# Performance work log

Hardware: AMD Instinct MI355X
Metric: run time of the kernel (lower is better)

Reference implementation:

```python
import jax, jax.numpy as jnp
import numpy as np

B, S, D, H = 4, 2048, 512, 8
KD = D // H          # key_dim == head_dim == 64
FFN = 4 * D

def _ln(x, g, b, eps):
    mu = x.mean(-1, keepdims=True)
    var = ((x - mu) ** 2).mean(-1, keepdims=True)
    return (x - mu) / jnp.sqrt(var + eps) * g + b

def setup_inputs():
    key = jax.random.key(0)
    ks = jax.random.split(key, 8)
    def lin(k, o, i, scale=0.02):
        k1, k2 = jax.random.split(k)
        return (jax.random.normal(k1, (o, i), jnp.float32) * scale,
                jax.random.normal(k2, (o,), jnp.float32) * scale)
    wq, bq = lin(ks[0], D, D)
    wk, bk = lin(ks[1], D, D)
    wv, bv = lin(ks[2], D, D)
    wg, bg = lin(ks[3], D, D)
    wo, bo = lin(ks[4], D, D)
    fc1_w, fc1_b = lin(ks[5], FFN, D)
    fc2_w, fc2_b = lin(ks[6], D, FFN)
    return {
        'src': jax.random.normal(ks[7], (B, S, D), jnp.float32),
        'mask': jnp.zeros((S, S), jnp.bool_),
        'padding_mask': jnp.zeros((B, S), jnp.bool_),
        'wq': wq, 'bq': bq, 'wk': wk, 'bk': bk, 'wv': wv, 'bv': bv,
        'wg': wg, 'bg': bg, 'wo': wo, 'bo': bo,
        'fc1_w': fc1_w, 'fc1_b': fc1_b, 'fc2_w': fc2_w, 'fc2_b': fc2_b,
        'ln_ffn_g': jnp.ones((FFN,), jnp.float32), 'ln_ffn_b': jnp.zeros((FFN,), jnp.float32),
        'n0_g': jnp.ones((D,), jnp.float32), 'n0_b': jnp.zeros((D,), jnp.float32),
        'n1_g': jnp.ones((D,), jnp.float32), 'n1_b': jnp.zeros((D,), jnp.float32),
    }

def reference(src, mask, padding_mask, wq, bq, wk, bk, wv, bv, wg, bg, wo, bo,
              fc1_w, fc1_b, fc2_w, fc2_b, ln_ffn_g, ln_ffn_b, n0_g, n0_b, n1_g, n1_b):
    b, s, d = src.shape
    # RetNet per-head decay mask (h, s, s): exp((i-j)*log(gamma_h)) on the lower triangle,
    # row-normalized by sqrt(row sum) (torchscale RetNetRelPos, parallel mode).
    idx = jnp.arange(s)
    diff = (idx[:, None] - idx[None, :]).astype(src.dtype)
    decay = jnp.log(1.0 - 2.0 ** (-5.0 - jnp.arange(H, dtype=src.dtype)))
    dm = jnp.where(diff[None] >= 0, jnp.exp(diff[None] * decay[:, None, None]), 0.0)
    dm = dm / jnp.sqrt(dm.sum(-1, keepdims=True))
    # projections; k scaled by key_dim**-0.5 before head split
    q = (src @ wq.T + bq).reshape(b, s, H, KD).transpose(0, 2, 1, 3)
    k = ((src @ wk.T + bk) * (KD ** -0.5)).reshape(b, s, H, KD).transpose(0, 2, 1, 3)
    v = src @ wv.T + bv
    g = src @ wg.T + bg
    # parallel retention: additive decay bias, detached L1 row normalization
    qk = jnp.einsum('bhid,bhjd->bhij', q, k) + dm[None]
    den = jnp.maximum(jnp.abs(jax.lax.stop_gradient(qk).sum(-1, keepdims=True)), 1.0)
    qk = qk / den
    vr = v.reshape(b, s, H, KD).transpose(0, 2, 1, 3)
    o = jnp.einsum('bhij,bhjd->bhid', qk, vr).transpose(0, 2, 1, 3)  # (b,s,h,hd)
    # per-head LayerNorm, eps=1e-6, no affine
    mu = o.mean(-1, keepdims=True)
    o = (o - mu) / jnp.sqrt(((o - mu) ** 2).mean(-1, keepdims=True) + 1e-6)
    o = jax.nn.silu(g) * o.reshape(b, s, d)
    o = o @ wo.T + bo
    # post-norm residual layout
    x = _ln(src + o, n0_g, n0_b, 1e-5)
    h = jax.nn.gelu(x @ fc1_w.T + fc1_b, approximate=False)
    h = _ln(h, ln_ffn_g, ln_ffn_b, 1e-6)  # subln
    h = h @ fc2_w.T + fc2_b
    return _ln(x + h, n1_g, n1_b, 1e-5)
```

## Files before the change

### kernel.cpp

```cpp
#include <hip/hip_runtime.h>
#include <hip/hip_bf16.h>
#include <math.h>

#define DEV __device__ __forceinline__

typedef __attribute__((ext_vector_type(4))) float f32x4;
typedef __attribute__((ext_vector_type(16))) float f32x16;
typedef __attribute__((ext_vector_type(8))) short bf16x8;
typedef __attribute__((ext_vector_type(8))) unsigned short u16x8;
typedef unsigned short u16;
typedef unsigned int u32;

DEV u16 f2bf(float f) {
  union { float f; u32 u; } v; v.f = f;
  u32 r = v.u + 0x7fffu + ((v.u >> 16) & 1u);
  return (u16)(r >> 16);
}
DEV float bf2f(u16 h) {
  union { u32 u; float f; } v; v.u = ((u32)h) << 16;
  return v.f;
}
DEV float bfel(bf16x8 v, int e) {
  union { bf16x8 b; u16x8 u; } x; x.b = v; return bf2f(x.u[e]);
}

DEV void gl_lds16(const u16* g, u16* s) {
  __builtin_amdgcn_global_load_lds((const __attribute__((address_space(1))) void*)g,
                                   (__attribute__((address_space(3))) void*)s, 16, 0, 0);
}

DEV void barrier_() {
  __builtin_amdgcn_sched_barrier(0);
  asm volatile("" ::: "memory");
  __builtin_amdgcn_s_barrier();
  asm volatile("" ::: "memory");
  __builtin_amdgcn_sched_barrier(0);
}

#define MFMA16(a, b, c) __builtin_amdgcn_mfma_f32_16x16x32_bf16((a), (b), (c), 0, 0, 0)
#define MFMA32(a, b, c) __builtin_amdgcn_mfma_f32_32x32x16_bf16((a), (b), (c), 0, 0, 0)

DEV void cast8(const float* in, u16* out, float s) {
  f32x4 a = *(const f32x4*)in;
  f32x4 b = *(const f32x4*)(in + 4);
  u16x8 r;
  r[0] = f2bf(a[0] * s); r[1] = f2bf(a[1] * s); r[2] = f2bf(a[2] * s); r[3] = f2bf(a[3] * s);
  r[4] = f2bf(b[0] * s); r[5] = f2bf(b[1] * s); r[6] = f2bf(b[2] * s); r[7] = f2bf(b[3] * s);
  *(u16x8*)out = r;
}

__global__ __launch_bounds__(256) void prep_cast(
    const float* __restrict__ src, const float* __restrict__ wq, const float* __restrict__ wk,
    const float* __restrict__ wv, const float* __restrict__ wg, const float* __restrict__ wo,
    const float* __restrict__ fc1, const float* __restrict__ fc2,
    const float* __restrict__ bq, const float* __restrict__ bk,
    const float* __restrict__ bv, const float* __restrict__ bg,
    u16* __restrict__ src_bf, u16* __restrict__ Wcat, u16* __restrict__ wo_bf,
    u16* __restrict__ fc1_bf, u16* __restrict__ fc2_bf, float* __restrict__ bcat) {
  int u = blockIdx.x * 256 + threadIdx.x;
  if (u < 524288) {
    cast8(src + (size_t)u * 8, src_bf + (size_t)u * 8, 1.0f);
  } else if (u < 557056) {
    int v = u - 524288; cast8(wq + (size_t)v * 8, Wcat + (size_t)v * 8, 1.0f);
  } else if (u < 589824) {
    int v = u - 557056; cast8(wk + (size_t)v * 8, Wcat + 262144 + (size_t)v * 8, 0.125f);
  } else if (u < 622592) {
    int v = u - 589824; cast8(wv + (size_t)v * 8, Wcat + 524288 + (size_t)v * 8, 1.0f);
  } else if (u < 655360) {
    int v = u - 622592; cast8(wg + (size_t)v * 8, Wcat + 786432 + (size_t)v * 8, 1.0f);
  } else if (u < 688128) {
    int v = u - 655360; cast8(wo + (size_t)v * 8, wo_bf + (size_t)v * 8, 1.0f);
  } else if (u < 819200) {
    int v = u - 688128; cast8(fc1 + (size_t)v * 8, fc1_bf + (size_t)v * 8, 1.0f);
  } else if (u < 950272) {
    int v = u - 819200; cast8(fc2 + (size_t)v * 8, fc2_bf + (size_t)v * 8, 1.0f);
  } else if (u < 950528) {
    int v = u - 950272;
    #pragma unroll
    for (int e = 0; e < 8; e++) {
      int c = v * 8 + e;
      float val;
      if (c < 512)       val = bq[c];
      else if (c < 1024) val = bk[c - 512] * 0.125f;
      else if (c < 1536) val = bv[c - 1024];
      else               val = bg[c - 1536];
      bcat[c] = val;
    }
  }
}

template <int ACT>
__global__ __launch_bounds__(256) void gemm_ring(
    const u16* __restrict__ A, const u16* __restrict__ W, const float* __restrict__ bias,
    u16* __restrict__ Ob, int N, int K, int TN) {
  __shared__ __align__(16) u16 sm[32768];
  const int t = threadIdx.x, l = t & 63;
  const int w = t >> 6, wr = (w >> 1) * 64, wc = (w & 1) * 64;
  const int lc = l & 15, lch = l >> 4;
  const int NT = K >> 5;

  const int orig = blockIdx.x;
  const int cpx = gridDim.x >> 3;
  const int sid = (orig & 7) * cpx + (orig >> 3);
  const int bm = (sid / TN) * 128, bn = (sid % TN) * 128;

  const int srow = t >> 2, sc = t & 3;
  const int soff = (sc ^ ((srow >> 1) & 3)) * 8;
  const u16* stA = A + (size_t)(bm + srow) * K + soff;
  const u16* stB = W + (size_t)(bn + srow) * K + soff;
  const size_t rstep = (size_t)64 * K;

#define STAGE(tile)                                       \
  {                                                       \
    u16* d = sm + ((tile) & 3) * 8192 + t * 8;            \
    const int kt = (tile) * 32;                           \
    gl_lds16(stA + kt, d);                                \
    gl_lds16(stA + rstep + kt, d + 2048);                 \
    gl_lds16(stB + kt, d + 4096);                         \
    gl_lds16(stB + rstep + kt, d + 6144);                 \
  }

  f32x4 acc[4][4] = {};
  STAGE(0) STAGE(1) STAGE(2)

  const int key = (lch ^ ((lc >> 1) & 3)) * 8;
  for (int tt = 0; tt < NT; ++tt) {
    const int rem = NT - 1 - tt;
    if (rem >= 3) {
      STAGE(tt + 3)
      asm volatile("s_waitcnt vmcnt(12)" ::: "memory");
    } else if (rem == 2) {
      asm volatile("s_waitcnt vmcnt(8)" ::: "memory");
    } else if (rem == 1) {
      asm volatile("s_waitcnt vmcnt(4)" ::: "memory");
    } else {
      asm volatile("s_waitcnt vmcnt(0)" ::: "memory");
    }
    barrier_();
    const u16* bufp = sm + (tt & 3) * 8192;
    bf16x8 af[4], bfv[4];
    #pragma unroll
    for (int mi = 0; mi < 4; mi++)
      af[mi] = *(const bf16x8*)&bufp[(wr + mi * 16 + lc) * 32 + key];
    #pragma unroll
    for (int ni = 0; ni < 4; ni++)
      bfv[ni] = *(const bf16x8*)&bufp[4096 + (wc + ni * 16 + lc) * 32 + key];
    #pragma unroll
    for (int mi = 0; mi < 4; mi++)
      #pragma unroll
      for (int ni = 0; ni < 4; ni++)
        acc[mi][ni] = MFMA16(af[mi], bfv[ni], acc[mi][ni]);
    asm volatile("s_waitcnt lgkmcnt(0)" ::: "memory");
    barrier_();
  }
#undef STAGE

  u16* osm = sm;
  #pragma unroll
  for (int ni = 0; ni < 4; ni++) {
    const int col = wc + ni * 16 + lc;
    const float bb = bias[bn + col];
    const int ckey = col >> 3, clow = col & 7;
    #pragma unroll
    for (int mi = 0; mi < 4; mi++) {
      #pragma unroll
      for (int r = 0; r < 4; r++) {
        const int row = wr + mi * 16 + lch * 4 + r;
        float v = acc[mi][ni][r] + bb;
        if (ACT == 1) v = 0.5f * v * (1.0f + erff(v * 0.70710678118f));
        osm[row * 128 + ((ckey ^ ((row & 7) << 1)) << 3) + clow] = f2bf(v);
      }
    }
  }
  __syncthreads();
  #pragma unroll
  for (int p = 0; p < 8; p++) {
    const int flat = p * 256 + t;
    const int row = flat >> 4, c = flat & 15;
    u16x8 y = *(const u16x8*)&osm[row * 128 + ((c ^ ((row & 7) << 1)) << 3)];
    *(u16x8*)&Ob[(size_t)(bm + row) * N + bn + c * 8] = y;
  }
}

template <int ACT>
__global__ __launch_bounds__(256) void gemm_m64_ring(
    const u16* __restrict__ A, const u16* __restrict__ W, const float* __restrict__ bias,
    u16* __restrict__ Ob, int N, int K, int TN) {
  __shared__ __align__(16) u16 sm[24576];
  const int t = threadIdx.x, l = t & 63;
  const int w = t >> 6, wr = (w >> 1) * 32, wc = (w & 1) * 64;
  const int lc = l & 15, lch = l >> 4;
  const int NT = K >> 5;

  const int orig = blockIdx.x;
  const int cpx = gridDim.x >> 3;
  const int sid = (orig & 7) * cpx + (orig >> 3);
  const int bm = (sid / TN) * 64, bn = (sid % TN) * 128;

  const int srow = t >> 2, sc = t & 3;
  const int soff = (sc ^ ((srow >> 1) & 3)) * 8;
  const u16* stA = A + (size_t)(bm + srow) * K + soff;
  const u16* stB = W + (size_t)(bn + srow) * K + soff;
  const size_t rstep = (size_t)64 * K;

#define STAGE(tile)                                       \
  {                                                       \
    u16* d = sm + ((tile) & 3) * 6144 + t * 8;            \
    const int kt = (tile) * 32;                           \
    gl_lds16(stA + kt, d);                                \
    gl_lds16(stB + kt, d + 2048);                         \
    gl_lds16(stB + rstep + kt, d + 4096);                 \
  }

  f32x4 acc[2][4] = {};
  STAGE(0) STAGE(1) STAGE(2)

  const int key = (lch ^ ((lc >> 1) & 3)) * 8;
  for (int tt = 0; tt < NT; ++tt) {
    const int rem = NT - 1 - tt;
    if (rem >= 3) {
      STAGE(tt + 3)
      asm volatile("s_waitcnt vmcnt(9)" ::: "memory");
    } else if (rem == 2) {
      asm volatile("s_waitcnt vmcnt(6)" ::: "memory");
    } else if (rem == 1) {
      asm volatile("s_waitcnt vmcnt(3)" ::: "memory");
    } else {
      asm volatile("s_waitcnt vmcnt(0)" ::: "memory");
    }
    barrier_();
    const u16* bufp = sm + (tt & 3) * 6144;
    bf16x8 af[2], bfv[4];
    #pragma unroll
    for (int mi = 0; mi < 2; mi++)
      af[mi] = *(const bf16x8*)&bufp[(wr + mi * 16 + lc) * 32 + key];
    #pragma unroll
    for (int ni = 0; ni < 4; ni++)
      bfv[ni] = *(const bf16x8*)&bufp[2048 + (wc + ni * 16 + lc) * 32 + key];
    #pragma unroll
    for (int mi = 0; mi < 2; mi++)
      #pragma unroll
      for (int ni = 0; ni < 4; ni++)
        acc[mi][ni] = MFMA16(af[mi], bfv[ni], acc[mi][ni]);
    asm volatile("s_waitcnt lgkmcnt(0)" ::: "memory");
    barrier_();
  }
#undef STAGE

  u16* osm = sm;
  #pragma unroll
  for (int ni = 0; ni < 4; ni++) {
    const int col = wc + ni * 16 + lc;
    const float bb = bias[bn + col];
    const int ckey = col >> 3, clow = col & 7;
    #pragma unroll
    for (int mi = 0; mi < 2; mi++) {
      #pragma unroll
      for (int r = 0; r < 4; r++) {
        const int row = wr + mi * 16 + lch * 4 + r;
        float v = acc[mi][ni][r] + bb;
        if (ACT == 1) v = 0.5f * v * (1.0f + erff(v * 0.70710678118f));
        osm[row * 128 + ((ckey ^ ((row & 7) << 1)) << 3) + clow] = f2bf(v);
      }
    }
  }
  __syncthreads();
  #pragma unroll
  for (int p = 0; p < 4; p++) {
    const int flat = p * 256 + t;
    const int row = flat >> 4, c = flat & 15;
    u16x8 y = *(const u16x8*)&osm[row * 128 + ((c ^ ((row & 7) << 1)) << 3)];
    *(u16x8*)&Ob[(size_t)(bm + row) * N + bn + c * 8] = y;
  }
}

__global__ __launch_bounds__(256) void transkv(
    const u16* __restrict__ qkvg, u16* __restrict__ ktg, u16* __restrict__ vtg,
    float* __restrict__ Wtab) {
  __shared__ u16 Lk[64 * 72], Lv[64 * 72];
  const int t = threadIdx.x;
  const int bh = blockIdx.x, c = blockIdx.y, b = bh >> 3, h = bh & 7;
  const int jt = c * 64;
  const u16* kptr = qkvg + (size_t)(b * 2048 + jt) * 2048 + 512 + h * 64;
  const u16* vptr = kptr + 512;
  const int r0 = t >> 3, c0 = (t & 7) * 8;
  u16x8 k0 = *(const u16x8*)(kptr + (size_t)r0 * 2048 + c0);
  u16x8 k1 = *(const u16x8*)(kptr + (size_t)(r0 + 32) * 2048 + c0);
  u16x8 v0 = *(const u16x8*)(vptr + (size_t)r0 * 2048 + c0);
  u16x8 v1 = *(const u16x8*)(vptr + (size_t)(r0 + 32) * 2048 + c0);
  #pragma unroll
  for (int e = 0; e < 8; e++) {
    Lk[(c0 + e) * 72 + r0] = k0[e];  Lk[(c0 + e) * 72 + 32 + r0] = k1[e];
    Lv[(c0 + e) * 72 + r0] = v0[e];  Lv[(c0 + e) * 72 + 32 + r0] = v1[e];
  }
  __syncthreads();
  {
    u16* kd = ktg + (size_t)bh * 64 * 2048 + jt;
    u16* vd = vtg + (size_t)bh * 64 * 2048 + jt;
    *(u16x8*)(kd + (size_t)r0 * 2048 + c0)        = *(const u16x8*)&Lk[r0 * 72 + c0];
    *(u16x8*)(kd + (size_t)(r0 + 32) * 2048 + c0) = *(const u16x8*)&Lk[(r0 + 32) * 72 + c0];
    *(u16x8*)(vd + (size_t)r0 * 2048 + c0)        = *(const u16x8*)&Lv[r0 * 72 + c0];
    *(u16x8*)(vd + (size_t)(r0 + 32) * 2048 + c0) = *(const u16x8*)&Lv[(r0 + 32) * 72 + c0];
  }
  if (t < 64) {
    const float gamma = 1.0f - exp2f(-5.0f - (float)h);
    float acc = 0.0f, p = 1.0f;
    for (int jj = 0; jj < 64; jj++) {
      acc += p * bf2f(Lv[t * 72 + (63 - jj)]);
      p *= gamma;
    }
    Wtab[((size_t)bh * 32 + c) * 64 + t] = acc;
  }
}

__global__ __launch_bounds__(256) void scan_kernel(
    const u16* __restrict__ ktg, float* __restrict__ Ctab, float* __restrict__ ksum) {
  __shared__ float ps[4][64];
  const int t = threadIdx.x, bh = blockIdx.x, h = bh & 7;
  const int a = t & 63, q = t >> 6;
  const u16* kr = ktg + (size_t)bh * 64 * 2048 + (size_t)a * 2048 + q * 512;
  float s = 0.0f;
  for (int j = 0; j < 512; j += 8) {
    u16x8 v = *(const u16x8*)(kr + j);
    #pragma unroll
    for (int e = 0; e < 8; e++) s += bf2f(v[e]);
  }
  ps[q][a] = s;
  __syncthreads();
  if (t < 64) {
    ksum[bh * 64 + t] = ps[0][t] + ps[1][t] + ps[2][t] + ps[3][t];
    const float gamma = 1.0f - exp2f(-5.0f - (float)h);
    const float g64 = exp2f(64.0f * log2f(gamma));
    float* Wp = Ctab + (size_t)bh * 32 * 64 + t;
    float C = 0.0f;
    for (int c = 0; c < 32; c++) {
      C = C * g64 + Wp[c * 64];
      Wp[c * 64] = C;
    }
  }
}

__global__ __launch_bounds__(256) void vtk_kernel(
    const u16* __restrict__ vtg, const u16* __restrict__ ktg, u16* __restrict__ vtk) {
  __shared__ float red[3][4096];
  const int t = threadIdx.x, l = t & 63, w = t >> 6;
  const int bh = blockIdx.x;
  const int lc = l & 15, lch = l >> 4;
  const u16* vb = vtg + (size_t)bh * 64 * 2048;
  const u16* kb = ktg + (size_t)bh * 64 * 2048;
  f32x4 acc[4][4] = {};
  for (int it = 0; it < 16; ++it) {
    const int j0 = w * 512 + it * 32 + lch * 8;
    bf16x8 af[4], bfr[4];
    #pragma unroll
    for (int mt = 0; mt < 4; mt++)
      af[mt] = *(const bf16x8*)(vb + (size_t)(mt * 16 + lc) * 2048 + j0);
    #pragma unroll
    for (int nt = 0; nt < 4; nt++)
      bfr[nt] = *(const bf16x8*)(kb + (size_t)(nt * 16 + lc) * 2048 + j0);
    #pragma unroll
    for (int mt = 0; mt < 4; mt++)
      #pragma unroll
      for (int nt = 0; nt < 4; nt++)
        acc[mt][nt] = MFMA16(af[mt], bfr[nt], acc[mt][nt]);
  }
  if (w > 0) {
    #pragma unroll
    for (int mt = 0; mt < 4; mt++)
      #pragma unroll
      for (int nt = 0; nt < 4; nt++)
        #pragma unroll
        for (int r = 0; r < 4; r++)
          red[w - 1][(mt * 16 + lch * 4 + r) * 64 + nt * 16 + lc] = acc[mt][nt][r];
  }
  __syncthreads();
  if (w == 0) {
    u16* out = vtk + (size_t)bh * 64 * 64;
    #pragma unroll
    for (int mt = 0; mt < 4; mt++)
      #pragma unroll
      for (int nt = 0; nt < 4; nt++)
        #pragma unroll
        for (int r = 0; r < 4; r++) {
          int row = mt * 16 + lch * 4 + r, col = nt * 16 + lc;
          float v = acc[mt][nt][r] + red[0][row * 64 + col] + red[1][row * 64 + col] +
                    red[2][row * 64 + col];
          out[row * 64 + col] = f2bf(v);
        }
  }
}

__global__ __launch_bounds__(512) void ret_out(
    const u16* __restrict__ qkvg, const u16* __restrict__ vtg,
    const u16* __restrict__ vtk, const float* __restrict__ Ctab,
    const float* __restrict__ ksum, u16* __restrict__ gated) {
  const int S = 2048, DD = 2048;
  const int bh = blockIdx.x, b = bh >> 3, h = bh & 7;
  const int t = threadIdx.x, l = t & 63, w = t >> 6;
  const int lid = l & 31, hi = l >> 5;
  const int wrow = blockIdx.y * 256 + w * 32;
  const int i_q = wrow + lid;
  const int chunk = wrow >> 6;
  const int iloc = i_q & 63;

  __shared__ __align__(16) u16 sm[18432];
  float* smf = (float*)sm;

  const size_t base = (size_t)b * S * DD + (size_t)h * 64;
  const u16* qp = qkvg + base;
  const u16* gp = qkvg + base + 1536;

  const float gamma = 1.0f - exp2f(-5.0f - (float)h);
  const float l2g = log2f(gamma);
  const float rowsum = (1.0f - exp2f((float)(i_q + 1) * l2g)) * exp2f(5.0f + (float)h);
  const float rrs = rsqrtf(rowsum);

  {
    const int il = t >> 3, j0 = (t & 7) * 8;
    u16x8 row;
    #pragma unroll
    for (int e = 0; e < 8; e++) {
      int d = il - (j0 + e);
      row[e] = (d >= 0) ? f2bf(exp2f((float)d * l2g)) : (u16)0;
    }
    *(u16x8*)&sm[il * 72 + j0] = row;
  }
  if (t < 256) {
    int cc = blockIdx.y * 4 - 1 + (t >> 6);
    smf[4608 + t] = (cc >= 0) ? Ctab[((size_t)bh * 32 + cc) * 64 + (t & 63)] : 0.0f;
  } else if (t < 320) {
    smf[4864 + (t - 256)] = ksum[bh * 64 + (t - 256)];
  }
  __syncthreads();

  bf16x8 qf[4];
  #pragma unroll
  for (int kc = 0; kc < 4; kc++)
    qf[kc] = *(const bf16x8*)(qp + (size_t)i_q * DD + kc * 16 + 8 * hi);

  const u16* vt_b = vtg + (size_t)bh * 64 * S;
  const u16* vk_b = vtk + (size_t)bh * 64 * 64;

  f32x16 accO0, accO1;
  #pragma unroll
  for (int r = 0; r < 16; r++) { accO0[r] = 0.0f; accO1[r] = 0.0f; }

  #pragma unroll
  for (int kc = 0; kc < 4; kc++) {
    bf16x8 lb = *(const bf16x8*)&sm[iloc * 72 + kc * 16 + hi * 8];
    bf16x8 va0 = *(const bf16x8*)(vt_b + (size_t)lid * S + chunk * 64 + kc * 16 + hi * 8);
    bf16x8 va1 = *(const bf16x8*)(vt_b + (size_t)(lid + 32) * S + chunk * 64 + kc * 16 + hi * 8);
    accO0 = MFMA32(va0, lb, accO0);
    accO1 = MFMA32(va1, lb, accO1);
  }
  {
    const float gpw = exp2f((float)(iloc + 1) * l2g);
    const float* Cst = &smf[4608 + (w >> 1) * 64];
    #pragma unroll
    for (int r = 0; r < 16; r++) {
      int br = (r & 3) + 8 * (r >> 2) + 4 * hi;
      accO0[r] += gpw * Cst[br];
      accO1[r] += gpw * Cst[32 + br];
    }
  }
  #pragma unroll
  for (int r = 0; r < 16; r++) { accO0[r] *= rrs; accO1[r] *= rrs; }
  #pragma unroll
  for (int kc = 0; kc < 4; kc++) {
    bf16x8 ka0 = *(const bf16x8*)(vk_b + (size_t)lid * 64 + kc * 16 + hi * 8);
    bf16x8 ka1 = *(const bf16x8*)(vk_b + (size_t)(lid + 32) * 64 + kc * 16 + hi * 8);
    accO0 = MFMA32(ka0, qf[kc], accO0);
    accO1 = MFMA32(ka1, qf[kc], accO1);
  }
  float dsum = 0.0f;
  #pragma unroll
  for (int kc = 0; kc < 4; kc++) {
    const float* Ks = &smf[4864 + kc * 16 + hi * 8];
    #pragma unroll
    for (int e = 0; e < 8; e++) dsum += bfel(qf[kc], e) * Ks[e];
  }
  dsum += __shfl_xor(dsum, 32);
  float den = dsum + sqrtf(rowsum);
  float rden = 1.0f / fmaxf(fabsf(den), 1.0f);

  float o0[16], o1[16];
  float s1 = 0.0f, s2 = 0.0f;
  #pragma unroll
  for (int r = 0; r < 16; r++) {
    o0[r] = accO0[r] * rden; s1 += o0[r]; s2 += o0[r] * o0[r];
    o1[r] = accO1[r] * rden; s1 += o1[r]; s2 += o1[r] * o1[r];
  }
  s1 += __shfl_xor(s1, 32);
  s2 += __shfl_xor(s2, 32);
  float mu = s1 * (1.0f / 64.0f);
  float var = s2 * (1.0f / 64.0f) - mu * mu;
  float rv = rsqrtf(var + 1e-6f);

  __syncthreads();

  u16* Ot = sm + w * 2304;
  #pragma unroll
  for (int r = 0; r < 16; r++) {
    int d = (r & 3) + 8 * (r >> 2) + 4 * hi;
    Ot[lid * 72 + d]      = f2bf((o0[r] - mu) * rv);
    Ot[lid * 72 + 32 + d] = f2bf((o1[r] - mu) * rv);
  }
  {
    const int i2 = l >> 1, half = l & 1;
    const int row = wrow + i2;
    #pragma unroll
    for (int c = 0; c < 4; c++) {
      u16x8 y8 = *(const u16x8*)&Ot[i2 * 72 + half * 32 + c * 8];
      u16x8 g8 = *(const u16x8*)(gp + (size_t)row * DD + half * 32 + c * 8);
      u16x8 o8;
      #pragma unroll
      for (int e = 0; e < 8; e++) {
        float gv = bf2f(g8[e]);
        float sg = gv / (1.0f + __expf(-gv));
        o8[e] = f2bf(bf2f(y8[e]) * sg);
      }
      *(u16x8*)&gated[((size_t)(b * S + row)) * 512 + h * 64 + half * 32 + c * 8] = o8;
    }
  }
}

template <int AF32, int WF>
__global__ __launch_bounds__(256) void add_lnT(
    const void* __restrict__ Ap, const u16* __restrict__ Bv,
    const float* __restrict__ gam, const float* __restrict__ bet, float eps,
    float* __restrict__ Of, u16* __restrict__ Ob) {
  int row = blockIdx.x * 4 + (threadIdx.x >> 6);
  int l = threadIdx.x & 63;
  float x[8];
  u16x8 cv = *(const u16x8*)(Bv + (size_t)row * 512 + l * 8);
  if (AF32) {
    const float* a = (const float*)Ap + (size_t)row * 512 + l * 8;
    f32x4 a0 = *(const f32x4*)a, a1 = *(const f32x4*)(a + 4);
    #pragma unroll
    for (int e = 0; e < 4; e++) { x[e] = a0[e] + bf2f(cv[e]); x[4 + e] = a1[e] + bf2f(cv[4 + e]); }
  } else {
    u16x8 av = *(const u16x8*)((const u16*)Ap + (size_t)row * 512 + l * 8);
    #pragma unroll
    for (int e = 0; e < 8; e++) x[e] = bf2f(av[e]) + bf2f(cv[e]);
  }
  float s = 0.f, s2 = 0.f;
  #pragma unroll
  for (int e = 0; e < 8; e++) { s += x[e]; s2 += x[e] * x[e]; }
  #pragma unroll
  for (int m = 1; m <= 32; m <<= 1) { s += __shfl_xor(s, m); s2 += __shfl_xor(s2, m); }
  float mu = s * (1.0f / 512.0f);
  float var = s2 * (1.0f / 512.0f) - mu * mu;
  float rinv = rsqrtf(var + eps);
  f32x4 g0 = *(const f32x4*)(gam + l * 8), g1 = *(const f32x4*)(gam + l * 8 + 4);
  f32x4 b0 = *(const f32x4*)(bet + l * 8), b1 = *(const f32x4*)(bet + l * 8 + 4);
  f32x4 y0, y1;
  #pragma unroll
  for (int e = 0; e < 4; e++) {
    y0[e] = (x[e] - mu) * rinv * g0[e] + b0[e];
    y1[e] = (x[4 + e] - mu) * rinv * g1[e] + b1[e];
  }
  if (WF) {
    float* op = Of + (size_t)row * 512 + l * 8;
    *(f32x4*)op = y0;
    *(f32x4*)(op + 4) = y1;
  }
  if (Ob) {
    u16x8 rb_;
    #pragma unroll
    for (int e = 0; e < 4; e++) { rb_[e] = f2bf(y0[e]); rb_[4 + e] = f2bf(y1[e]); }
    *(u16x8*)(Ob + (size_t)row * 512 + l * 8) = rb_;
  }
}

__global__ __launch_bounds__(256) void subln_ffn(
    u16* __restrict__ hbuf, const float* __restrict__ gam, const float* __restrict__ bet) {
  int row = blockIdx.x * 4 + (threadIdx.x >> 6);
  int l = threadIdx.x & 63;
  u16* p = hbuf + (size_t)row * 2048;
  float x[32];
  #pragma unroll
  for (int cch = 0; cch < 4; cch++) {
    u16x8 v = *(const u16x8*)(p + cch * 512 + l * 8);
    #pragma unroll
    for (int e = 0; e < 8; e++) x[cch * 8 + e] = bf2f(v[e]);
  }
  float s = 0.f, s2 = 0.f;
  #pragma unroll
  for (int e = 0; e < 32; e++) { s += x[e]; s2 += x[e] * x[e]; }
  #pragma unroll
  for (int m = 1; m <= 32; m <<= 1) { s += __shfl_xor(s, m); s2 += __shfl_xor(s2, m); }
  float mu = s * (1.0f / 2048.0f);
  float var = s2 * (1.0f / 2048.0f) - mu * mu;
  float rinv = rsqrtf(var + 1e-6f);
  #pragma unroll
  for (int cch = 0; cch < 4; cch++) {
    int col = cch * 512 + l * 8;
    f32x4 g0 = *(const f32x4*)(gam + col), g1 = *(const f32x4*)(gam + col + 4);
    f32x4 b0 = *(const f32x4*)(bet + col), b1 = *(const f32x4*)(bet + col + 4);
    u16x8 o;
    #pragma unroll
    for (int e = 0; e < 4; e++) {
      o[e]     = f2bf((x[cch * 8 + e]     - mu) * rinv * g0[e] + b0[e]);
      o[4 + e] = f2bf((x[cch * 8 + 4 + e] - mu) * rinv * g1[e] + b1[e]);
    }
    *(u16x8*)(p + col) = o;
  }
}

extern "C" void kernel_launch(void* const* d_in, const int* in_sizes, int n_in,
                              void* d_out, int out_size, void* d_ws, size_t ws_size,
                              hipStream_t stream) {
  const float* src  = (const float*)d_in[0];
  const float* wq   = (const float*)d_in[3];
  const float* bq   = (const float*)d_in[4];
  const float* wk   = (const float*)d_in[5];
  const float* bk   = (const float*)d_in[6];
  const float* wv   = (const float*)d_in[7];
  const float* bv   = (const float*)d_in[8];
  const float* wg   = (const float*)d_in[9];
  const float* bg   = (const float*)d_in[10];
  const float* wo   = (const float*)d_in[11];
  const float* bo   = (const float*)d_in[12];
  const float* fc1w = (const float*)d_in[13];
  const float* fc1b = (const float*)d_in[14];
  const float* fc2w = (const float*)d_in[15];
  const float* fc2b = (const float*)d_in[16];
  const float* lng  = (const float*)d_in[17];
  const float* lnb  = (const float*)d_in[18];
  const float* n0g  = (const float*)d_in[19];
  const float* n0b  = (const float*)d_in[20];
  const float* n1g  = (const float*)d_in[21];
  const float* n1b  = (const float*)d_in[22];

  if (ws_size < 91242496u) return;

  char* ws = (char*)d_ws;
  u16*   src_bf = (u16*)(ws + 0);
  u16*   Wcat   = (u16*)(ws + 8388608);
  u16*   wo_bf  = (u16*)(ws + 10485760);
  u16*   fc1_bf = (u16*)(ws + 11010048);
  u16*   fc2_bf = (u16*)(ws + 13107200);
  float* bcat   = (float*)(ws + 15204352);
  u16*   qkvg   = (u16*)(ws + 15212544);
  u16*   gated  = (u16*)(ws + 48766976);
  u16*   attn   = (u16*)(ws + 57155584);
  u16*   vtg    = (u16*)(ws + 65544192);
  u16*   ktg    = (u16*)(ws + 73932800);
  u16*   xbf    = (u16*)(ws + 82321408);
  float* Ctab   = (float*)(ws + 90710016);
  u16*   vtkb   = (u16*)(ws + 90972160);
  float* ksumb  = (float*)(ws + 91234304);

  prep_cast<<<3713, 256, 0, stream>>>(src, wq, wk, wv, wg, wo, fc1w, fc2w,
                                      bq, bk, bv, bg,
                                      src_bf, Wcat, wo_bf, fc1_bf, fc2_bf, bcat);
  gemm_ring<0><<<1024, 256, 0, stream>>>(src_bf, Wcat, bcat, qkvg, 2048, 512, 16);
  transkv<<<dim3(32, 32), 256, 0, stream>>>(qkvg, ktg, vtg, Ctab);
  scan_kernel<<<32, 256, 0, stream>>>(ktg, Ctab, ksumb);
  vtk_kernel<<<32, 256, 0, stream>>>(vtg, ktg, vtkb);
  ret_out<<<dim3(32, 8), 512, 0, stream>>>(qkvg, vtg, vtkb, Ctab, ksumb, gated);
  gemm_m64_ring<0><<<512, 256, 0, stream>>>(gated, wo_bf, bo, attn, 512, 512, 4);
  add_lnT<1, 0><<<2048, 256, 0, stream>>>(src, attn, n0g, n0b, 1e-5f, nullptr, xbf);
  gemm_ring<1><<<1024, 256, 0, stream>>>(xbf, fc1_bf, fc1b, qkvg, 2048, 512, 16);
  subln_ffn<<<2048, 256, 0, stream>>>(qkvg, lng, lnb);
  gemm_m64_ring<0><<<512, 256, 0, stream>>>(qkvg, fc2_bf, fc2b, attn, 512, 2048, 4);
  add_lnT<0, 1><<<2048, 256, 0, stream>>>(xbf, attn, n1g, n1b, 1e-5f, (float*)d_out, nullptr);
}
```

Before: 194.9 us.

## Replace 128x128 ring GEMM with 256x256 double-buffered 512-thread GEMM

The QKVG and FC1 GEMMs (M=8192, N=2048, K=512) now use 256x256 output tiles with 8 waves, a BK of 64 and a two-stage LDS double buffer in place of the four-deep 128x128 ring. Each wave computes 128x64, which raises arithmetic intensity per LDS load and cuts the grid from 1024 to 256 blocks, one per CU. The MFMA section is raised to a higher wave priority. The trade-off is 128KB of LDS, fewer waves in flight, only 8 K-iterations with a full vmcnt(0) wait each step, and a single wave of blocks with no tail balancing.

```diff
diff --git a/kernel.cpp b/kernel.cpp
--- a/kernel.cpp
+++ b/kernel.cpp
@@ -90,94 +90,93 @@
 }
 
 template <int ACT>
-__global__ __launch_bounds__(256) void gemm_ring(
+__global__ __launch_bounds__(512) void gemm_256(
     const u16* __restrict__ A, const u16* __restrict__ W, const float* __restrict__ bias,
     u16* __restrict__ Ob, int N, int K, int TN) {
-  __shared__ __align__(16) u16 sm[32768];
+  __shared__ __align__(16) u16 sm[65536];
   const int t = threadIdx.x, l = t & 63;
-  const int w = t >> 6, wr = (w >> 1) * 64, wc = (w & 1) * 64;
+  const int w = t >> 6, wm = w >> 2, wn = w & 3;
   const int lc = l & 15, lch = l >> 4;
-  const int NT = K >> 5;
+  const int NT = K >> 6;
 
   const int orig = blockIdx.x;
   const int cpx = gridDim.x >> 3;
   const int sid = (orig & 7) * cpx + (orig >> 3);
-  const int bm = (sid / TN) * 128, bn = (sid % TN) * 128;
-
-  const int srow = t >> 2, sc = t & 3;
-  const int soff = (sc ^ ((srow >> 1) & 3)) * 8;
+  const int bm = (sid / TN) * 256, bn = (sid % TN) * 256;
+
+  const int srow = t >> 3, sch = t & 7;
+  const int soff = (sch ^ (srow & 7)) * 8;
   const u16* stA = A + (size_t)(bm + srow) * K + soff;
   const u16* stB = W + (size_t)(bn + srow) * K + soff;
   const size_t rstep = (size_t)64 * K;
 
-#define STAGE(tile)                                       \
-  {                                                       \
-    u16* d = sm + ((tile) & 3) * 8192 + t * 8;            \
-    const int kt = (tile) * 32;                           \
-    gl_lds16(stA + kt, d);                                \
-    gl_lds16(stA + rstep + kt, d + 2048);                 \
-    gl_lds16(stB + kt, d + 4096);                         \
-    gl_lds16(stB + rstep + kt, d + 6144);                 \
-  }
-
-  f32x4 acc[4][4] = {};
-  STAGE(0) STAGE(1) STAGE(2)
-
-  const int key = (lch ^ ((lc >> 1) & 3)) * 8;
+#define STAGE(bidx, kt)                                        \
+  {                                                            \
+    u16* d = sm + (bidx) * 32768 + t * 8;                      \
+    _Pragma("unroll")                                          \
+    for (int j = 0; j < 4; j++) {                              \
+      gl_lds16(stA + (size_t)j * rstep + (kt), d + j * 4096);  \
+      gl_lds16(stB + (size_t)j * rstep + (kt), d + 16384 + j * 4096); \
+    }                                                          \
+  }
+
+  f32x4 acc[8][4] = {};
+  STAGE(0, 0)
+  asm volatile("s_waitcnt vmcnt(0)" ::: "memory");
+  barrier_();
+
   for (int tt = 0; tt < NT; ++tt) {
-    const int rem = NT - 1 - tt;
-    if (rem >= 3) {
-      STAGE(tt + 3)
-      asm volatile("s_waitcnt vmcnt(12)" ::: "memory");
-    } else if (rem == 2) {
-      asm volatile("s_waitcnt vmcnt(8)" ::: "memory");
-    } else if (rem == 1) {
-      asm volatile("s_waitcnt vmcnt(4)" ::: "memory");
-    } else {
-      asm volatile("s_waitcnt vmcnt(0)" ::: "memory");
-    }
+    if (tt + 1 < NT) STAGE((tt + 1) & 1, (tt + 1) * 64)
+    const u16* Ar = sm + (tt & 1) * 32768;
+    const u16* Br = Ar + 16384;
+    #pragma unroll
+    for (int ks = 0; ks < 2; ks++) {
+      bf16x8 bfv[4];
+      #pragma unroll
+      for (int ni = 0; ni < 4; ni++) {
+        const int r = wn * 64 + ni * 16 + lc;
+        bfv[ni] = *(const bf16x8*)&Br[r * 64 + (((ks * 4 + lch) ^ (r & 7)) * 8)];
+      }
+      __builtin_amdgcn_s_setprio(1);
+      #pragma unroll
+      for (int mi = 0; mi < 8; mi++) {
+        const int r = wm * 128 + mi * 16 + lc;
+        bf16x8 af = *(const bf16x8*)&Ar[r * 64 + (((ks * 4 + lch) ^ (r & 7)) * 8)];
+        #pragma unroll
+        for (int ni = 0; ni < 4; ni++)
+          acc[mi][ni] = MFMA16(af, bfv[ni], acc[mi][ni]);
+      }
+      __builtin_amdgcn_s_setprio(0);
+    }
+    asm volatile("s_waitcnt lgkmcnt(0)" ::: "memory");
+    asm volatile("s_waitcnt vmcnt(0)" ::: "memory");
     barrier_();
-    const u16* bufp = sm + (tt & 3) * 8192;
-    bf16x8 af[4], bfv[4];
-    #pragma unroll
-    for (int mi = 0; mi < 4; mi++)
-      af[mi] = *(const bf16x8*)&bufp[(wr + mi * 16 + lc) * 32 + key];
-    #pragma unroll
-    for (int ni = 0; ni < 4; ni++)
-      bfv[ni] = *(const bf16x8*)&bufp[4096 + (wc + ni * 16 + lc) * 32 + key];
-    #pragma unroll
-    for (int mi = 0; mi < 4; mi++)
-      #pragma unroll
-      for (int ni = 0; ni < 4; ni++)
-        acc[mi][ni] = MFMA16(af[mi], bfv[ni], acc[mi][ni]);
-    asm volatile("s_waitcnt lgkmcnt(0)" ::: "memory");
-    barrier_();
   }
 #undef STAGE
 
   u16* osm = sm;
   #pragma unroll
   for (int ni = 0; ni < 4; ni++) {
-    const int col = wc + ni * 16 + lc;
+    const int col = wn * 64 + ni * 16 + lc;
     const float bb = bias[bn + col];
-    const int ckey = col >> 3, clow = col & 7;
-    #pragma unroll
-    for (int mi = 0; mi < 4; mi++) {
+    const int cch = col >> 3, clow = col & 7;
+    #pragma unroll
+    for (int mi = 0; mi < 8; mi++) {
       #pragma unroll
       for (int r = 0; r < 4; r++) {
-        const int row = wr + mi * 16 + lch * 4 + r;
+        const int row = wm * 128 + mi * 16 + lch * 4 + r;
         float v = acc[mi][ni][r] + bb;
         if (ACT == 1) v = 0.5f * v * (1.0f + erff(v * 0.70710678118f));
-        osm[row * 128 + ((ckey ^ ((row & 7) << 1)) << 3) + clow] = f2bf(v);
+        osm[row * 256 + ((cch ^ ((row & 7) << 2)) << 3) + clow] = f2bf(v);
       }
     }
   }
   __syncthreads();
   #pragma unroll
-  for (int p = 0; p < 8; p++) {
-    const int flat = p * 256 + t;
-    const int row = flat >> 4, c = flat & 15;
-    u16x8 y = *(const u16x8*)&osm[row * 128 + ((c ^ ((row & 7) << 1)) << 3)];
+  for (int p = 0; p < 16; p++) {
+    const int flat = p * 512 + t;
+    const int row = flat >> 5, c = flat & 31;
+    u16x8 y = *(const u16x8*)&osm[row * 256 + ((c ^ ((row & 7) << 2)) << 3)];
     *(u16x8*)&Ob[(size_t)(bm + row) * N + bn + c * 8] = y;
   }
 }
@@ -654,14 +653,14 @@
   prep_cast<<<3713, 256, 0, stream>>>(src, wq, wk, wv, wg, wo, fc1w, fc2w,
                                       bq, bk, bv, bg,
                                       src_bf, Wcat, wo_bf, fc1_bf, fc2_bf, bcat);
-  gemm_ring<0><<<1024, 256, 0, stream>>>(src_bf, Wcat, bcat, qkvg, 2048, 512, 16);
+  gemm_256<0><<<256, 512, 0, stream>>>(src_bf, Wcat, bcat, qkvg, 2048, 512, 8);
   transkv<<<dim3(32, 32), 256, 0, stream>>>(qkvg, ktg, vtg, Ctab);
   scan_kernel<<<32, 256, 0, stream>>>(ktg, Ctab, ksumb);
   vtk_kernel<<<32, 256, 0, stream>>>(vtg, ktg, vtkb);
   ret_out<<<dim3(32, 8), 512, 0, stream>>>(qkvg, vtg, vtkb, Ctab, ksumb, gated);
   gemm_m64_ring<0><<<512, 256, 0, stream>>>(gated, wo_bf, bo, attn, 512, 512, 4);
   add_lnT<1, 0><<<2048, 256, 0, stream>>>(src, attn, n0g, n0b, 1e-5f, nullptr, xbf);
-  gemm_ring<1><<<1024, 256, 0, stream>>>(xbf, fc1_bf, fc1b, qkvg, 2048, 512, 16);
+  gemm_256<1><<<256, 512, 0, stream>>>(xbf, fc1_bf, fc1b, qkvg, 2048, 512, 8);
   subln_ffn<<<2048, 256, 0, stream>>>(qkvg, lng, lnb);
   gemm_m64_ring<0><<<512, 256, 0, stream>>>(qkvg, fc2_bf, fc2b, attn, 512, 2048, 4);
   add_lnT<0, 1><<<2048, 256, 0, stream>>>(xbf, attn, n1g, n1b, 1e-5f, (float*)d_out, nullptr);
```

After: 190.5 us. -2.2%, faster.
